# Performance work log

Measured on AMD Instinct MI355X. Metric: run time of the kernel, lower is better.

The kernel has to match this reference:

```python
import jax, jax.numpy as jnp
import numpy as np

B, S, HIST, D, NH, L = 8, 1024, 128, 1024, 16, 6
SD, TD, AD = 10, 3, 5
DH = D // NH
FF = 4 * D
EPS = 1e-5
SCALE = 1.0 / np.sqrt(DH)


def posenc(T):
    # sinusoidal PE, matches PositionalEncoding (positions start at 0)
    pos = jnp.arange(T, dtype=jnp.float32)[:, None]
    div = jnp.exp(jnp.arange(0, D, 2, dtype=jnp.float32) * (-np.log(10000.0) / D))
    pe = jnp.zeros((T, D), jnp.float32)
    pe = pe.at[:, 0::2].set(jnp.sin(pos * div))
    pe = pe.at[:, 1::2].set(jnp.cos(pos * div))
    return pe


def layernorm(x, g, b):
    m = jnp.mean(x, -1, keepdims=True)
    v = jnp.var(x, -1, keepdims=True)
    return (x - m) * jax.lax.rsqrt(v + EPS) * g + b


def mlp2(u, w1, b1, w2, b2):
    # Linear -> SiLU -> Linear (ConditionEmbedding branch)
    return jax.nn.silu(u @ w1 + b1) @ w2 + b2


def mha(q_in, kv_in, wq, bq, wk, bk, wv, bv, wo, bo, mask):
    Bq, Tq, _ = q_in.shape
    Tk = kv_in.shape[1]
    q = (q_in @ wq + bq).reshape(Bq, Tq, NH, DH)
    k = (kv_in @ wk + bk).reshape(Bq, Tk, NH, DH)
    v = (kv_in @ wv + bv).reshape(Bq, Tk, NH, DH)
    s = jnp.einsum('bthd,bshd->bhts', q, k) * SCALE + mask
    a = jax.nn.softmax(s, axis=-1)
    o = jnp.einsum('bhts,bshd->bthd', a, v).reshape(Bq, Tq, D)
    return o @ wo + bo


def setup_inputs():
    key = jax.random.key(0)
    ki = iter(jax.random.split(key, 64))
    w = lambda *sh: jax.random.normal(next(ki), sh, jnp.float32) * 0.02
    z = lambda *sh: jnp.zeros(sh, jnp.float32)
    inp = {
        'x': jax.random.normal(next(ki), (B, S, SD), jnp.float32),
        't': jax.random.randint(next(ki), (B,), 0, 30, dtype=jnp.int32),
        'target': jax.random.normal(next(ki), (B, TD), jnp.float32),
        'action': jax.random.normal(next(ki), (B, AD), jnp.float32),
        'history': jax.random.normal(next(ki), (B, HIST, SD), jnp.float32),
        'in_w': w(SD, D), 'in_b': z(D),
        't_w1': w(1, D), 't_b1': z(D), 't_w2': w(D, D), 't_b2': z(D),
        'tg_w1': w(TD, D), 'tg_b1': z(D), 'tg_w2': w(D, D), 'tg_b2': z(D),
        'ac_w1': w(AD, D), 'ac_b1': z(D), 'ac_w2': w(D, D), 'ac_b2': z(D),
        'sa_wq': w(L, D, D), 'sa_bq': z(L, D), 'sa_wk': w(L, D, D), 'sa_bk': z(L, D),
        'sa_wv': w(L, D, D), 'sa_bv': z(L, D), 'sa_wo': w(L, D, D), 'sa_bo': z(L, D),
        'ca_wq': w(L, D, D), 'ca_bq': z(L, D), 'ca_wk': w(L, D, D), 'ca_bk': z(L, D),
        'ca_wv': w(L, D, D), 'ca_bv': z(L, D), 'ca_wo': w(L, D, D), 'ca_bo': z(L, D),
        'ln1_g': jnp.ones((L, D), jnp.float32), 'ln1_b': z(L, D),
        'ln2_g': jnp.ones((L, D), jnp.float32), 'ln2_b': z(L, D),
        'ln3_g': jnp.ones((L, D), jnp.float32), 'ln3_b': z(L, D),
        'ff_w1': w(L, D, FF), 'ff_b1': z(L, FF), 'ff_w2': w(L, FF, D), 'ff_b2': z(L, D),
        'out_w': w(D, SD), 'out_b': z(SD),
    }
    return inp


def reference(x, t, target, action, history, in_w, in_b,
              t_w1, t_b1, t_w2, t_b2, tg_w1, tg_b1, tg_w2, tg_b2,
              ac_w1, ac_b1, ac_w2, ac_b2,
              sa_wq, sa_bq, sa_wk, sa_bk, sa_wv, sa_bv, sa_wo, sa_bo,
              ca_wq, ca_bq, ca_wk, ca_bk, ca_wv, ca_bv, ca_wo, ca_bo,
              ln1_g, ln1_b, ln2_g, ln2_b, ln3_g, ln3_b,
              ff_w1, ff_b1, ff_w2, ff_b2, out_w, out_b):
    # embed current traj and history (PE applied to each separately, as in torch code)
    x_emb = x @ in_w + in_b + posenc(S)[None]
    h_emb = history @ in_w + in_b + posenc(HIST)[None]
    # condition embedding: t + target + action branches
    cond = (mlp2(t[:, None].astype(jnp.float32), t_w1, t_b1, t_w2, t_b2)
            + mlp2(target, tg_w1, tg_b1, tg_w2, tg_b2)
            + mlp2(action, ac_w1, ac_b1, ac_w2, ac_b2))
    z = jnp.concatenate([h_emb, x_emb], axis=1) + cond[:, None, :]  # [B, T, D]
    T = HIST + S
    mask = jnp.where(jnp.tril(jnp.ones((T, T), bool)), 0.0, -jnp.inf)[None, None]
    mem = z  # TransformerDecoder memory is the (fixed) input sequence
    for i in range(L):
        # post-LN TransformerDecoderLayer: self-attn, cross-attn, relu FFN
        z = layernorm(z + mha(z, z, sa_wq[i], sa_bq[i], sa_wk[i], sa_bk[i],
                              sa_wv[i], sa_bv[i], sa_wo[i], sa_bo[i], mask), ln1_g[i], ln1_b[i])
        z = layernorm(z + mha(z, mem, ca_wq[i], ca_bq[i], ca_wk[i], ca_bk[i],
                              ca_wv[i], ca_bv[i], ca_wo[i], ca_bo[i], mask), ln2_g[i], ln2_b[i])
        ff = jax.nn.relu(z @ ff_w1[i] + ff_b1[i]) @ ff_w2[i] + ff_b2[i]
        z = layernorm(z + ff, ln3_g[i], ln3_b[i])
    return z[:, -S:, :] @ out_w + out_b
```

## Files before the change

### kernel.cpp

```cpp
#include <hip/hip_runtime.h>
#include <hip/hip_bf16.h>
#include <stdint.h>

#define B_    8
#define S_    1024
#define HIST_ 128
#define T_    1152
#define D_    1024
#define NH_   16
#define DH_   64
#define FF_   4096
#define L_    6
#define NROWS_ (B_*T_)

typedef __attribute__((ext_vector_type(8))) __bf16 bf16x8;
typedef __attribute__((ext_vector_type(4))) __bf16 bf16x4;
typedef __attribute__((ext_vector_type(4))) float  f32x4;

static __device__ __forceinline__ f32x4 mfma16(bf16x8 a, bf16x8 b, f32x4 c) {
  return __builtin_amdgcn_mfma_f32_16x16x32_bf16(a, b, c, 0, 0, 0);
}
static __device__ __forceinline__ void gload16(const __bf16* g, __bf16* l) {
  __builtin_amdgcn_global_load_lds((const __attribute__((address_space(1))) void*)g,
                                   (__attribute__((address_space(3))) void*)l, 16, 0, 0);
}
static __device__ __forceinline__ void gload16b(const char* g, char* l) {
  __builtin_amdgcn_global_load_lds((const __attribute__((address_space(1))) void*)g,
                                   (__attribute__((address_space(3))) void*)l, 16, 0, 0);
}
static __device__ __forceinline__ int xcd_swz(int orig, int nwg) {
  const int q = nwg >> 3, r = nwg & 7;
  const int x = orig & 7, i = orig >> 3;
  return (x < r ? x*(q+1) : r*(q+1) + (x-r)*q) + i;
}

template<int OUTMODE, int RELU>
__global__ __launch_bounds__(512, 2) void gemm256_k(const __bf16* __restrict__ A,
                                                    const __bf16* __restrict__ Bt,
                                                    const float* __restrict__ b1,
                                                    const float* __restrict__ b2,
                                                    const float* __restrict__ b3, int s1, int s2,
                                                    void* __restrict__ CoutRM,
                                                    __bf16* __restrict__ CoutT,
                                                    int M, int N, int K, int ldc, int tsplit) {
  __shared__ __align__(16) __bf16 Lds[2][2][2][8192];
  const int tid = threadIdx.x;
  const int wid = tid >> 6, ln = tid & 63;
  const int wm = wid >> 2, wn = wid & 3;
  const int l15 = ln & 15, g = ln >> 4;
  const int nbx = N >> 8;
  const int wg = xcd_swz(blockIdx.x, gridDim.x);
  const int m0 = (wg / nbx) << 8, n0 = (wg % nbx) << 8;
  const size_t rstep = (size_t)K * 2;

  const int srow = tid >> 2, schunk = tid & 3;
  const int sx = (schunk ^ ((srow >> 1) & 3)) << 4;
  const char* gAr = (const char*)A  + (size_t)(m0 + srow)*rstep + sx;
  const char* gBr = (const char*)Bt + (size_t)(n0 + srow)*rstep + sx;
  const size_t hstep = (size_t)128 * rstep;

  const int xr = (g ^ ((l15 >> 1) & 3)) << 4;
  const int arow = l15 * 64 + xr;
  const int aoffm = (wm*128 + 0) * 64;
  const int boff  = (wn*64) * 64;

  const f32x4 zero = {0.f,0.f,0.f,0.f};
  f32x4 acc[8][4];
#pragma unroll
  for (int i=0;i<8;i++)
#pragma unroll
    for (int j=0;j<4;j++) acc[i][j] = zero;

  auto stage4 = [&](int buf, int ks, int tile) {
    const size_t off = (size_t)tile*128 + (size_t)ks*64;
    char* la = (char*)&Lds[buf][ks][0][0];
    char* lb = (char*)&Lds[buf][ks][1][0];
    gload16b(gAr + off,         la + tid*16);
    gload16b(gAr + off + hstep, la + 8192 + tid*16);
    gload16b(gBr + off,         lb + tid*16);
    gload16b(gBr + off + hstep, lb + 8192 + tid*16);
  };

  auto ktile = [&](int buf, bool st, int stile, bool gate0) {
    if (gate0) { asm volatile("s_waitcnt vmcnt(0)" ::: "memory"); }
    else       { asm volatile("s_waitcnt vmcnt(8)" ::: "memory"); }
    __builtin_amdgcn_s_barrier();
    const char* As0 = (const char*)&Lds[buf][0][0][0];
    const char* Bs0 = (const char*)&Lds[buf][0][1][0];
    const char* As1 = (const char*)&Lds[buf][1][0][0];
    const char* Bs1 = (const char*)&Lds[buf][1][1][0];
    bf16x8 af[4], af2[4], bfr[4];
#pragma unroll
    for (int mi=0;mi<4;mi++) af[mi]  = *(const bf16x8*)(As0 + aoffm + mi*1024 + arow);
#pragma unroll
    for (int ni=0;ni<4;ni++) bfr[ni] = *(const bf16x8*)(Bs0 + boff + ni*1024 + arow);
    __builtin_amdgcn_s_setprio(1);
#pragma unroll
    for (int mi=0;mi<4;mi++)
#pragma unroll
      for (int ni=0;ni<4;ni++) acc[mi][ni] = mfma16(af[mi], bfr[ni], acc[mi][ni]);
    __builtin_amdgcn_s_setprio(0);
#pragma unroll
    for (int mi=0;mi<4;mi++) af2[mi] = *(const bf16x8*)(As0 + aoffm + 4096 + mi*1024 + arow);
    asm volatile("s_waitcnt lgkmcnt(0)" ::: "memory");
    __builtin_amdgcn_sched_barrier(0);
    __builtin_amdgcn_s_barrier();
    if (st) stage4(buf, 0, stile);
    __builtin_amdgcn_s_setprio(1);
#pragma unroll
    for (int mi=0;mi<4;mi++)
#pragma unroll
      for (int ni=0;ni<4;ni++) acc[4+mi][ni] = mfma16(af2[mi], bfr[ni], acc[4+mi][ni]);
    __builtin_amdgcn_s_setprio(0);
#pragma unroll
    for (int mi=0;mi<4;mi++) af[mi]  = *(const bf16x8*)(As1 + aoffm + mi*1024 + arow);
#pragma unroll
    for (int ni=0;ni<4;ni++) bfr[ni] = *(const bf16x8*)(Bs1 + boff + ni*1024 + arow);
    __builtin_amdgcn_s_setprio(1);
#pragma unroll
    for (int mi=0;mi<4;mi++)
#pragma unroll
      for (int ni=0;ni<4;ni++) acc[mi][ni] = mfma16(af[mi], bfr[ni], acc[mi][ni]);
    __builtin_amdgcn_s_setprio(0);
#pragma unroll
    for (int mi=0;mi<4;mi++) af2[mi] = *(const bf16x8*)(As1 + aoffm + 4096 + mi*1024 + arow);
    asm volatile("s_waitcnt lgkmcnt(0)" ::: "memory");
    __builtin_amdgcn_sched_barrier(0);
    __builtin_amdgcn_s_barrier();
    if (st) stage4(buf, 1, stile);
    __builtin_amdgcn_s_setprio(1);
#pragma unroll
    for (int mi=0;mi<4;mi++)
#pragma unroll
      for (int ni=0;ni<4;ni++) acc[4+mi][ni] = mfma16(af2[mi], bfr[ni], acc[4+mi][ni]);
    __builtin_amdgcn_s_setprio(0);
  };

  stage4(0, 0, 0); stage4(0, 1, 0);
  stage4(1, 0, 1); stage4(1, 1, 1);

  const int NT = K >> 6, NI = NT >> 1;
  for (int i = 0; i < NI; ++i) {
    const bool st = (i + 1 < NI);
    ktile(0, st, 2*i + 2, false);
    ktile(1, st, 2*i + 3, i == NI - 1);
  }

  const int colb = n0 + wn*64 + l15;
#pragma unroll
  for (int mi=0;mi<8;mi++) {
    const int row = m0 + wm*128 + mi*16 + g*4;
#pragma unroll
    for (int ni=0;ni<4;ni++) {
      const int col = colb + ni*16;
      const float bv = (col < s1) ? b1[col] : ((col < s2) ? b2[col-s1] : b3[col-s2]);
      if (OUTMODE == 3 && col >= tsplit) {
        bf16x4 ct;
#pragma unroll
        for (int j=0;j<4;j++) {
          float v = acc[mi][ni][j] + bv;
          if (RELU) v = fmaxf(v, 0.f);
          ct[j] = (__bf16)v;
        }
        *(bf16x4*)(CoutT + (size_t)(col - tsplit)*M + row) = ct;
      } else {
#pragma unroll
        for (int j=0;j<4;j++) {
          float v = acc[mi][ni][j] + bv;
          if (RELU) v = fmaxf(v, 0.f);
          if (OUTMODE == 0) ((float*)CoutRM)[(size_t)(row+j)*ldc + col] = v;
          else              ((__bf16*)CoutRM)[(size_t)(row+j)*ldc + col] = (__bf16)v;
        }
      }
    }
  }
}

__global__ __launch_bounds__(256) void attn_k(const __bf16* __restrict__ QK,
                                              const __bf16* __restrict__ Vt,
                                              __bf16* __restrict__ O) {
  __shared__ __align__(16) __bf16 Ks[2][4096];
  __shared__ __align__(16) __bf16 Vs[2][4096];
  __shared__ __align__(16) __bf16 Pl[4][32*72];
  const int tid = threadIdx.x;
  const int wv = tid >> 6, ln = tid & 63;
  const int l15 = ln & 15, g = ln >> 4;
  const int wg = xcd_swz(blockIdx.x, 1152);
  const int qb = 8 - (wg % 9);
  const int hd = (wg / 9) & 15;
  const int b  = wg / 144;
  const int q0 = qb*128 + wv*32;

  bf16x8 qf[2][2];
#pragma unroll
  for (int f=0; f<2; ++f)
#pragma unroll
    for (int h=0; h<2; ++h)
      qf[f][h] = *(const bf16x8*)(QK + (size_t)(b*T_ + q0 + f*16 + l15)*2048 + hd*64 + h*32 + g*8);

  const int sr = tid >> 3;
  const int si = tid & 7;
  const int cb0 = (si*16) ^ ((sr & 7) << 4);
  const char* kg = (const char*)(QK + (size_t)b*T_*2048 + 1024 + hd*64);
  const char* vg = (const char*)(Vt + (size_t)hd*64*NROWS_ + (size_t)b*T_);

  const f32x4 zero = {0.f,0.f,0.f,0.f};
  f32x4 o[2][4];
#pragma unroll
  for (int f=0; f<2; ++f)
#pragma unroll
    for (int d=0; d<4; ++d) o[f][d] = zero;
  float mrun[2] = {-3.0e38f, -3.0e38f};
  float lrun[2] = {0.f, 0.f};
  const int nt = 2*qb + 2;

  {
    const int c = 0, kt = 0;
#pragma unroll
    for (int hr=0; hr<2; ++hr) {
      const int r = sr + hr*32;
      gload16((const __bf16*)(kg + (size_t)(kt + r)*4096 + cb0), &Ks[c][0] + hr*2048 + wv*512);
      gload16((const __bf16*)(vg + (size_t)r*(NROWS_*2) + (size_t)kt*2 + cb0), &Vs[c][0] + hr*2048 + wv*512);
    }
  }

  for (int t = 0; t < nt; ++t) {
    __syncthreads();
    if (t+1 < nt) {
      const int c = (t+1)&1, kt2 = (t+1)*64;
#pragma unroll
      for (int hr=0; hr<2; ++hr) {
        const int r = sr + hr*32;
        gload16((const __bf16*)(kg + (size_t)(kt2 + r)*4096 + cb0), &Ks[c][0] + hr*2048 + wv*512);
        gload16((const __bf16*)(vg + (size_t)r*(NROWS_*2) + (size_t)kt2*2 + cb0), &Vs[c][0] + hr*2048 + wv*512);
      }
    }
    const int kt = t*64;
    if (kt > q0 + 31) continue;
    const char* ks = (const char*)&Ks[t&1][0];
    const char* vs = (const char*)&Vs[t&1][0];

#pragma unroll
    for (int f=0; f<2; ++f) {
      const int qrow = q0 + f*16 + l15;
      f32x4 st[4];
      __builtin_amdgcn_s_setprio(1);
#pragma unroll
      for (int kf=0; kf<4; ++kf) {
        const int row = kf*16 + l15;
        const int swz = (row & 7) << 4;
        const bf16x8 k0 = *(const bf16x8*)(ks + row*128 + ((g*16) ^ swz));
        const bf16x8 k1 = *(const bf16x8*)(ks + row*128 + ((64 + g*16) ^ swz));
        st[kf] = mfma16(k1, qf[f][1], mfma16(k0, qf[f][0], zero));
      }
      __builtin_amdgcn_s_setprio(0);
      float p[16];
#pragma unroll
      for (int kf=0; kf<4; ++kf)
#pragma unroll
        for (int r=0; r<4; ++r) {
          const int kgl = kt + kf*16 + g*4 + r;
          p[kf*4+r] = (kgl <= qrow) ? st[kf][r]*0.125f : -3.0e38f;
        }
      float mloc = p[0];
#pragma unroll
      for (int i=1;i<16;i++) mloc = fmaxf(mloc, p[i]);
      mloc = fmaxf(mloc, __shfl_xor(mloc, 16));
      mloc = fmaxf(mloc, __shfl_xor(mloc, 32));
      const float mnew = fmaxf(mrun[f], mloc);
      const float corr = __expf(mrun[f] - mnew);
      float ls = 0.f;
#pragma unroll
      for (int i=0;i<16;i++) { p[i] = __expf(p[i] - mnew); ls += p[i]; }
      ls += __shfl_xor(ls, 16); ls += __shfl_xor(ls, 32);
      lrun[f] = lrun[f]*corr + ls;
      mrun[f] = mnew;
#pragma unroll
      for (int kf=0; kf<4; ++kf) {
        bf16x4 pw;
#pragma unroll
        for (int r=0;r<4;r++) pw[r] = (__bf16)p[kf*4+r];
        *(bf16x4*)(&Pl[wv][(f*16 + l15)*72 + kf*16 + g*4]) = pw;
      }
      float cr[4];
#pragma unroll
      for (int r=0;r<4;r++) cr[r] = __shfl(corr, g*4 + r);
#pragma unroll
      for (int db=0; db<4; ++db)
#pragma unroll
        for (int r=0;r<4;r++) o[f][db][r] *= cr[r];
    }
    __builtin_amdgcn_s_setprio(1);
#pragma unroll
    for (int f=0; f<2; ++f)
#pragma unroll
      for (int ks2=0; ks2<2; ++ks2) {
        const bf16x8 pa = *(const bf16x8*)(&Pl[wv][(f*16 + l15)*72 + ks2*32 + g*8]);
#pragma unroll
        for (int db=0; db<4; ++db) {
          const int d = db*16 + l15;
          const bf16x8 vf = *(const bf16x8*)(vs + d*128 + ((ks2*64 + g*16) ^ ((d & 7) << 4)));
          o[f][db] = mfma16(pa, vf, o[f][db]);
        }
      }
    __builtin_amdgcn_s_setprio(0);
  }

#pragma unroll
  for (int f=0; f<2; ++f) {
    const float inv = 1.f / lrun[f];
    float ir[4];
#pragma unroll
    for (int r=0;r<4;r++) ir[r] = __shfl(inv, g*4 + r);
#pragma unroll
    for (int db=0; db<4; ++db)
#pragma unroll
      for (int r=0;r<4;r++)
        O[(size_t)(b*T_ + q0 + f*16 + g*4 + r)*D_ + hd*64 + db*16 + l15] = (__bf16)(o[f][db][r]*ir[r]);
  }
}

__global__ __launch_bounds__(256) void wprep_k(const float* __restrict__ q, const float* __restrict__ k,
                                               const float* __restrict__ v, const float* __restrict__ o,
                                               const float* __restrict__ cq, const float* __restrict__ ck,
                                               const float* __restrict__ cv, const float* __restrict__ co,
                                               const float* __restrict__ f1, const float* __restrict__ f2,
                                               __bf16* __restrict__ wb) {
  __shared__ float tile[32][33];
  const int id = blockIdx.x;
  const float* src; __bf16* dst; int R, C, bx, by;
  if (id < 8192) {
    const int m = id >> 10, t = id & 1023; bx = t & 31; by = t >> 5;
    const float* srcs[8] = {q,k,v,o,cq,ck,cv,co};
    src = srcs[m]; dst = wb + (size_t)m*1048576; R = 1024; C = 1024;
  } else if (id < 12288) {
    const int t = id - 8192; bx = t & 127; by = t >> 7;
    src = f1; dst = wb + (size_t)8*1048576; R = 1024; C = 4096;
  } else {
    const int t = id - 12288; bx = t & 31; by = t >> 5;
    src = f2; dst = wb + (size_t)12*1048576; R = 4096; C = 1024;
  }
  const int tx = threadIdx.x & 31, ty = threadIdx.x >> 5;
  const int r0 = by*32, c0 = bx*32;
#pragma unroll
  for (int i=0;i<4;i++) tile[ty+i*8][tx] = src[(size_t)(r0+ty+i*8)*C + c0+tx];
  __syncthreads();
#pragma unroll
  for (int i=0;i<4;i++) dst[(size_t)(c0+ty+i*8)*R + r0+tx] = (__bf16)tile[tx][ty+i*8];
}

__global__ __launch_bounds__(256) void ln_k(const float* __restrict__ zin, const float* __restrict__ yin,
                                            const float* __restrict__ gam, const float* __restrict__ bet,
                                            float* __restrict__ zout, __bf16* __restrict__ zbout) {
  const int row = blockIdx.x, tid = threadIdx.x;
  const f32x4 zv = ((const f32x4*)(zin + (size_t)row*D_))[tid];
  const f32x4 yv = ((const f32x4*)(yin + (size_t)row*D_))[tid];
  f32x4 v = zv + yv;
  float s1 = v[0]+v[1]+v[2]+v[3];
  float s2 = v[0]*v[0]+v[1]*v[1]+v[2]*v[2]+v[3]*v[3];
#pragma unroll
  for (int off=32; off; off>>=1) { s1 += __shfl_xor(s1,off); s2 += __shfl_xor(s2,off); }
  __shared__ float red[8];
  const int wv = tid>>6, ln = tid&63;
  if (ln==0) { red[wv] = s1; red[4+wv] = s2; }
  __syncthreads();
  s1 = red[0]+red[1]+red[2]+red[3];
  s2 = red[4]+red[5]+red[6]+red[7];
  const float mean = s1 * (1.f/1024.f);
  const float var = s2 * (1.f/1024.f) - mean*mean;
  const float rs = rsqrtf(var + 1e-5f);
  const f32x4 gv = ((const f32x4*)gam)[tid];
  const f32x4 bv = ((const f32x4*)bet)[tid];
  f32x4 r; bf16x4 rb;
#pragma unroll
  for (int j=0;j<4;j++) { float t = (v[j]-mean)*rs*gv[j] + bv[j]; r[j] = t; rb[j] = (__bf16)t; }
  ((f32x4*)(zout + (size_t)row*D_))[tid] = r;
  ((bf16x4*)(zbout + (size_t)row*D_))[tid] = rb;
}

__global__ __launch_bounds__(256) void cond1_k(const int* __restrict__ t, const float* __restrict__ target,
                                               const float* __restrict__ action,
                                               const float* __restrict__ t_w1, const float* __restrict__ t_b1,
                                               const float* __restrict__ tg_w1, const float* __restrict__ tg_b1,
                                               const float* __restrict__ ac_w1, const float* __restrict__ ac_b1,
                                               float* __restrict__ h3) {
  const int i = blockIdx.x*256 + threadIdx.x;
  const int b = i >> 10, d = i & 1023;
  float u = (float)t[b] * t_w1[d] + t_b1[d];
  h3[i] = u / (1.f + __expf(-u));
  u = tg_b1[d];
#pragma unroll
  for (int j=0;j<3;j++) u += target[b*3+j]*tg_w1[j*1024+d];
  h3[8192 + i] = u / (1.f + __expf(-u));
  u = ac_b1[d];
#pragma unroll
  for (int j=0;j<5;j++) u += action[b*5+j]*ac_w1[j*1024+d];
  h3[16384 + i] = u / (1.f + __expf(-u));
}

__global__ __launch_bounds__(256) void cond2_k(const float* __restrict__ h3,
                                               const float* __restrict__ t_w2, const float* __restrict__ tg_w2,
                                               const float* __restrict__ ac_w2, float* __restrict__ cpart) {
  const int i = blockIdx.x*256 + threadIdx.x;
  const int ks = blockIdx.y;
  const int b = i >> 10, d = i & 1023;
  const float* ht = h3 + b*1024;
  const float* hg = h3 + 8192 + b*1024;
  const float* ha = h3 + 16384 + b*1024;
  float a = 0.f;
  for (int k = ks*128; k < ks*128+128; ++k)
    a += ht[k]*t_w2[(size_t)k*1024+d] + hg[k]*tg_w2[(size_t)k*1024+d] + ha[k]*ac_w2[(size_t)k*1024+d];
  cpart[ks*8192 + i] = a;
}

__global__ __launch_bounds__(256) void embed_k(const float* __restrict__ x, const float* __restrict__ hist,
                                               const float* __restrict__ in_w, const float* __restrict__ in_b,
                                               const float* __restrict__ cpart,
                                               const float* __restrict__ t_b2, const float* __restrict__ tg_b2,
                                               const float* __restrict__ ac_b2,
                                               float* __restrict__ z, __bf16* __restrict__ zb,
                                               __bf16* __restrict__ memb) {
  const int row = blockIdx.x, tid = threadIdx.x;
  const int b = row / T_, tt = row - b*T_;
  const float* feat = (tt < HIST_) ? (hist + ((size_t)b*HIST_ + tt)*10) : (x + ((size_t)b*S_ + (tt-HIST_))*10);
  float f[10];
#pragma unroll
  for (int s=0;s<10;s++) f[s] = feat[s];
  const float te = (float)((tt < HIST_) ? tt : tt - HIST_);
  f32x4 a = ((const f32x4*)in_b)[tid];
#pragma unroll
  for (int u=0;u<2;u++) {
    const int d = tid*4 + 2*u;
    const float freq = __expf((float)d * (-9.210340371976184f/1024.f));
    float sn, cs;
    __sincosf(te*freq, &sn, &cs);
    a[2*u] += sn; a[2*u+1] += cs;
  }
  a += ((const f32x4*)t_b2)[tid];
  a += ((const f32x4*)tg_b2)[tid];
  a += ((const f32x4*)ac_b2)[tid];
  const int cb = b*256 + tid;
#pragma unroll
  for (int ks=0;ks<8;ks++) a += ((const f32x4*)cpart)[ks*2048 + cb];
#pragma unroll
  for (int s=0;s<10;s++) {
    const f32x4 wv = ((const f32x4*)(in_w + s*1024))[tid];
    a += wv * f[s];
  }
  ((f32x4*)(z + (size_t)row*D_))[tid] = a;
  bf16x4 ab;
#pragma unroll
  for (int j=0;j<4;j++) ab[j] = (__bf16)a[j];
  ((bf16x4*)(zb + (size_t)row*D_))[tid] = ab;
  ((bf16x4*)(memb + (size_t)row*D_))[tid] = ab;
}

__global__ __launch_bounds__(256) void outp_k(const float* __restrict__ z, const float* __restrict__ w,
                                              const float* __restrict__ bo, float* __restrict__ out) {
  const int wv = threadIdx.x>>6, ln = threadIdx.x&63;
  const int row = blockIdx.x*4 + wv;
  const int b = row >> 10, s = row & 1023;
  const float* zr = z + ((size_t)b*T_ + HIST_ + s)*D_;
  float acc[10];
#pragma unroll
  for (int o=0;o<10;o++) acc[o]=0.f;
  for (int k=ln; k<1024; k+=64) {
    const float zv = zr[k];
    const float* wr = w + k*10;
#pragma unroll
    for (int o=0;o<10;o++) acc[o] += zv*wr[o];
  }
#pragma unroll
  for (int o=0;o<10;o++) {
#pragma unroll
    for (int off=32; off; off>>=1) acc[o] += __shfl_xor(acc[o], off);
  }
  if (ln==0) {
#pragma unroll
    for (int o=0;o<10;o++) out[(size_t)row*10+o] = acc[o] + bo[o];
  }
}

extern "C" void kernel_launch(void* const* d_in, const int* in_sizes, int n_in,
                              void* d_out, int out_size, void* d_ws, size_t ws_size,
                              hipStream_t stream) {
  const float* x      = (const float*)d_in[0];
  const int*   t      = (const int*)  d_in[1];
  const float* target = (const float*)d_in[2];
  const float* action = (const float*)d_in[3];
  const float* hist   = (const float*)d_in[4];
  const float* in_w   = (const float*)d_in[5];
  const float* in_b   = (const float*)d_in[6];
  const float* t_w1   = (const float*)d_in[7];
  const float* t_b1   = (const float*)d_in[8];
  const float* t_w2   = (const float*)d_in[9];
  const float* t_b2   = (const float*)d_in[10];
  const float* tg_w1  = (const float*)d_in[11];
  const float* tg_b1  = (const float*)d_in[12];
  const float* tg_w2  = (const float*)d_in[13];
  const float* tg_b2  = (const float*)d_in[14];
  const float* ac_w1  = (const float*)d_in[15];
  const float* ac_b1  = (const float*)d_in[16];
  const float* ac_w2  = (const float*)d_in[17];
  const float* ac_b2  = (const float*)d_in[18];
  const float* sa_wq  = (const float*)d_in[19];
  const float* sa_bq  = (const float*)d_in[20];
  const float* sa_wk  = (const float*)d_in[21];
  const float* sa_bk  = (const float*)d_in[22];
  const float* sa_wv  = (const float*)d_in[23];
  const float* sa_bv  = (const float*)d_in[24];
  const float* sa_wo  = (const float*)d_in[25];
  const float* sa_bo  = (const float*)d_in[26];
  const float* ca_wq  = (const float*)d_in[27];
  const float* ca_bq  = (const float*)d_in[28];
  const float* ca_wk  = (const float*)d_in[29];
  const float* ca_bk  = (const float*)d_in[30];
  const float* ca_wv  = (const float*)d_in[31];
  const float* ca_bv  = (const float*)d_in[32];
  const float* ca_wo  = (const float*)d_in[33];
  const float* ca_bo  = (const float*)d_in[34];
  const float* ln1_g  = (const float*)d_in[35];
  const float* ln1_b  = (const float*)d_in[36];
  const float* ln2_g  = (const float*)d_in[37];
  const float* ln2_b  = (const float*)d_in[38];
  const float* ln3_g  = (const float*)d_in[39];
  const float* ln3_b  = (const float*)d_in[40];
  const float* ff_w1  = (const float*)d_in[41];
  const float* ff_b1  = (const float*)d_in[42];
  const float* ff_w2  = (const float*)d_in[43];
  const float* ff_b2  = (const float*)d_in[44];
  const float* out_w  = (const float*)d_in[45];
  const float* out_b  = (const float*)d_in[46];

  if (ws_size < (size_t)224*1024*1024) return;

  char* p = (char*)d_ws;
  auto take = [&](size_t bytes) { char* r = p; p += (bytes + 255) & ~(size_t)255; return r; };
  __bf16* wbuf = (__bf16*)take((size_t)16*1024*1024*2);
  float*  z    = (float*) take((size_t)NROWS_*D_*4);
  __bf16* zb   = (__bf16*)take((size_t)NROWS_*D_*2);
  __bf16* memb = (__bf16*)take((size_t)NROWS_*D_*2);
  __bf16* qk   = (__bf16*)take((size_t)NROWS_*2048*2);
  __bf16* vt   = (__bf16*)take((size_t)1024*NROWS_*2);
  __bf16* ob   = (__bf16*)take((size_t)NROWS_*D_*2);
  float*  y    = (float*) take((size_t)NROWS_*D_*4);
  float*  h3   = (float*) take((size_t)3*8192*4);
  float*  cpart= (float*) take((size_t)8*8192*4);
  __bf16* ffh  = qk;

  const dim3 blk(256);
  const dim3 blk5(512);
  const int BIG = 1<<30;
  cond1_k<<<32, blk, 0, stream>>>(t, target, action, t_w1, t_b1, tg_w1, tg_b1, ac_w1, ac_b1, h3);
  cond2_k<<<dim3(32,8), blk, 0, stream>>>(h3, t_w2, tg_w2, ac_w2, cpart);
  embed_k<<<NROWS_, blk, 0, stream>>>(x, hist, in_w, in_b, cpart, t_b2, tg_b2, ac_b2, z, zb, memb);

  const int M = NROWS_;
  for (int li=0; li<L_; ++li) {
    const size_t w0 = (size_t)li*D_*D_, b0 = (size_t)li*D_;
    const size_t f1 = (size_t)li*D_*FF_, fb1 = (size_t)li*FF_;
    wprep_k<<<16384, blk, 0, stream>>>(sa_wq+w0, sa_wk+w0, sa_wv+w0, sa_wo+w0,
                                       ca_wq+w0, ca_wk+w0, ca_wv+w0, ca_wo+w0,
                                       ff_w1+f1, ff_w2+f1, wbuf);
    gemm256_k<3,0><<<36*12, blk5, 0, stream>>>(zb, wbuf+0*1048576, sa_bq+b0, sa_bk+b0, sa_bv+b0, 1024, 2048,
                                               qk, vt, M, 3072, 1024, 2048, 2048);
    attn_k<<<1152, blk, 0, stream>>>(qk, vt, ob);
    gemm256_k<0,0><<<36*4, blk5, 0, stream>>>(ob, wbuf+3*1048576, sa_bo+b0, sa_bo+b0, sa_bo+b0, BIG, BIG,
                                              y, vt, M, 1024, 1024, 1024, BIG);
    ln_k<<<NROWS_, blk, 0, stream>>>(z, y, ln1_g+b0, ln1_b+b0, z, zb);
    gemm256_k<1,0><<<36*4, blk5, 0, stream>>>(zb, wbuf+4*1048576, ca_bq+b0, ca_bq+b0, ca_bq+b0, BIG, BIG,
                                              qk, vt, M, 1024, 1024, 2048, BIG);
    gemm256_k<3,0><<<36*8, blk5, 0, stream>>>(memb, wbuf+5*1048576, ca_bk+b0, ca_bv+b0, ca_bv+b0, 1024, 2048,
                                              qk + 1024, vt, M, 2048, 1024, 2048, 1024);
    attn_k<<<1152, blk, 0, stream>>>(qk, vt, ob);
    gemm256_k<0,0><<<36*4, blk5, 0, stream>>>(ob, wbuf+7*1048576, ca_bo+b0, ca_bo+b0, ca_bo+b0, BIG, BIG,
                                              y, vt, M, 1024, 1024, 1024, BIG);
    ln_k<<<NROWS_, blk, 0, stream>>>(z, y, ln2_g+b0, ln2_b+b0, z, zb);
    gemm256_k<1,1><<<36*16, blk5, 0, stream>>>(zb, wbuf+(size_t)8*1048576, ff_b1+fb1, ff_b1+fb1, ff_b1+fb1, BIG, BIG,
                                               ffh, vt, M, 4096, 1024, 4096, BIG);
    gemm256_k<0,0><<<36*4, blk5, 0, stream>>>(ffh, wbuf+(size_t)12*1048576, ff_b2+b0, ff_b2+b0, ff_b2+b0, BIG, BIG,
                                              y, vt, M, 1024, 4096, 1024, BIG);
    ln_k<<<NROWS_, blk, 0, stream>>>(z, y, ln3_g+b0, ln3_b+b0, z, zb);
  }
  outp_k<<<2048, blk, 0, stream>>>(z, out_w, out_b, (float*)d_out);
}
```

Baseline: 4.494 ms.

## Fuse cross-attn Q/KV GEMMs, reorder LDS fragment loads, add lazy softmax rescale

The GEMM kernel gains a second A pointer chosen by output column, so the cross-attention Q projection (from zb) and the K/V projection (from memb) run as one N=3072 launch instead of two. The GEMM k-tile loop now loads all A/B fragments for both half-tiles into separate registers ahead of the MFMAs and drops sched_barriers, aiming to overlap LDS reads with compute at the cost of more VGPRs. In attention, when no row's max grows by more than 8, the old max is kept and the output rescale is skipped (lazy rescaling), which cuts exp and multiply work but lets the unnormalised values grow by up to e^8.

```diff
diff --git a/kernel.cpp b/kernel.cpp
--- a/kernel.cpp
+++ b/kernel.cpp
@@ -36,6 +36,7 @@
 
 template<int OUTMODE, int RELU>
 __global__ __launch_bounds__(512, 2) void gemm256_k(const __bf16* __restrict__ A,
+                                                    const __bf16* __restrict__ A2, int asplit,
                                                     const __bf16* __restrict__ Bt,
                                                     const float* __restrict__ b1,
                                                     const float* __restrict__ b2,
@@ -52,16 +53,17 @@
   const int wg = xcd_swz(blockIdx.x, gridDim.x);
   const int m0 = (wg / nbx) << 8, n0 = (wg % nbx) << 8;
   const size_t rstep = (size_t)K * 2;
+  const __bf16* Aeff = (n0 < asplit) ? A : A2;
 
   const int srow = tid >> 2, schunk = tid & 3;
   const int sx = (schunk ^ ((srow >> 1) & 3)) << 4;
-  const char* gAr = (const char*)A  + (size_t)(m0 + srow)*rstep + sx;
-  const char* gBr = (const char*)Bt + (size_t)(n0 + srow)*rstep + sx;
+  const char* gAr = (const char*)Aeff + (size_t)(m0 + srow)*rstep + sx;
+  const char* gBr = (const char*)Bt   + (size_t)(n0 + srow)*rstep + sx;
   const size_t hstep = (size_t)128 * rstep;
 
   const int xr = (g ^ ((l15 >> 1) & 3)) << 4;
   const int arow = l15 * 64 + xr;
-  const int aoffm = (wm*128 + 0) * 64;
+  const int aoffm = (wm*128) * 64;
   const int boff  = (wn*64) * 64;
 
   const f32x4 zero = {0.f,0.f,0.f,0.f};
@@ -89,50 +91,48 @@
     const char* Bs0 = (const char*)&Lds[buf][0][1][0];
     const char* As1 = (const char*)&Lds[buf][1][0][0];
     const char* Bs1 = (const char*)&Lds[buf][1][1][0];
-    bf16x8 af[4], af2[4], bfr[4];
-#pragma unroll
-    for (int mi=0;mi<4;mi++) af[mi]  = *(const bf16x8*)(As0 + aoffm + mi*1024 + arow);
-#pragma unroll
-    for (int ni=0;ni<4;ni++) bfr[ni] = *(const bf16x8*)(Bs0 + boff + ni*1024 + arow);
+    bf16x8 a0[4], a1[4], b0[4], a2[4], b1v[4], a3[4];
+#pragma unroll
+    for (int mi=0;mi<4;mi++) a0[mi] = *(const bf16x8*)(As0 + aoffm + mi*1024 + arow);
+#pragma unroll
+    for (int ni=0;ni<4;ni++) b0[ni] = *(const bf16x8*)(Bs0 + boff + ni*1024 + arow);
+#pragma unroll
+    for (int mi=0;mi<4;mi++) a1[mi] = *(const bf16x8*)(As0 + aoffm + 4096 + mi*1024 + arow);
     __builtin_amdgcn_s_setprio(1);
 #pragma unroll
     for (int mi=0;mi<4;mi++)
 #pragma unroll
-      for (int ni=0;ni<4;ni++) acc[mi][ni] = mfma16(af[mi], bfr[ni], acc[mi][ni]);
+      for (int ni=0;ni<4;ni++) acc[mi][ni] = mfma16(a0[mi], b0[ni], acc[mi][ni]);
     __builtin_amdgcn_s_setprio(0);
 #pragma unroll
-    for (int mi=0;mi<4;mi++) af2[mi] = *(const bf16x8*)(As0 + aoffm + 4096 + mi*1024 + arow);
+    for (int mi=0;mi<4;mi++) a2[mi]  = *(const bf16x8*)(As1 + aoffm + mi*1024 + arow);
+#pragma unroll
+    for (int ni=0;ni<4;ni++) b1v[ni] = *(const bf16x8*)(Bs1 + boff + ni*1024 + arow);
     asm volatile("s_waitcnt lgkmcnt(0)" ::: "memory");
-    __builtin_amdgcn_sched_barrier(0);
     __builtin_amdgcn_s_barrier();
     if (st) stage4(buf, 0, stile);
     __builtin_amdgcn_s_setprio(1);
 #pragma unroll
     for (int mi=0;mi<4;mi++)
 #pragma unroll
-      for (int ni=0;ni<4;ni++) acc[4+mi][ni] = mfma16(af2[mi], bfr[ni], acc[4+mi][ni]);
+      for (int ni=0;ni<4;ni++) acc[4+mi][ni] = mfma16(a1[mi], b0[ni], acc[4+mi][ni]);
     __builtin_amdgcn_s_setprio(0);
 #pragma unroll
-    for (int mi=0;mi<4;mi++) af[mi]  = *(const bf16x8*)(As1 + aoffm + mi*1024 + arow);
-#pragma unroll
-    for (int ni=0;ni<4;ni++) bfr[ni] = *(const bf16x8*)(Bs1 + boff + ni*1024 + arow);
+    for (int mi=0;mi<4;mi++) a3[mi] = *(const bf16x8*)(As1 + aoffm + 4096 + mi*1024 + arow);
     __builtin_amdgcn_s_setprio(1);
 #pragma unroll
     for (int mi=0;mi<4;mi++)
 #pragma unroll
-      for (int ni=0;ni<4;ni++) acc[mi][ni] = mfma16(af[mi], bfr[ni], acc[mi][ni]);
+      for (int ni=0;ni<4;ni++) acc[mi][ni] = mfma16(a2[mi], b1v[ni], acc[mi][ni]);
     __builtin_amdgcn_s_setprio(0);
-#pragma unroll
-    for (int mi=0;mi<4;mi++) af2[mi] = *(const bf16x8*)(As1 + aoffm + 4096 + mi*1024 + arow);
     asm volatile("s_waitcnt lgkmcnt(0)" ::: "memory");
-    __builtin_amdgcn_sched_barrier(0);
     __builtin_amdgcn_s_barrier();
     if (st) stage4(buf, 1, stile);
     __builtin_amdgcn_s_setprio(1);
 #pragma unroll
     for (int mi=0;mi<4;mi++)
 #pragma unroll
-      for (int ni=0;ni<4;ni++) acc[4+mi][ni] = mfma16(af2[mi], bfr[ni], acc[4+mi][ni]);
+      for (int ni=0;ni<4;ni++) acc[4+mi][ni] = mfma16(a3[mi], b1v[ni], acc[4+mi][ni]);
     __builtin_amdgcn_s_setprio(0);
   };
 
@@ -267,14 +267,29 @@
       for (int i=1;i<16;i++) mloc = fmaxf(mloc, p[i]);
       mloc = fmaxf(mloc, __shfl_xor(mloc, 16));
       mloc = fmaxf(mloc, __shfl_xor(mloc, 32));
-      const float mnew = fmaxf(mrun[f], mloc);
-      const float corr = __expf(mrun[f] - mnew);
-      float ls = 0.f;
-#pragma unroll
-      for (int i=0;i<16;i++) { p[i] = __expf(p[i] - mnew); ls += p[i]; }
-      ls += __shfl_xor(ls, 16); ls += __shfl_xor(ls, 32);
-      lrun[f] = lrun[f]*corr + ls;
-      mrun[f] = mnew;
+      if (__all(mloc - mrun[f] <= 8.f)) {
+        float ls = 0.f;
+#pragma unroll
+        for (int i=0;i<16;i++) { p[i] = __expf(p[i] - mrun[f]); ls += p[i]; }
+        ls += __shfl_xor(ls, 16); ls += __shfl_xor(ls, 32);
+        lrun[f] += ls;
+      } else {
+        const float mnew = fmaxf(mrun[f], mloc);
+        const float corr = __expf(mrun[f] - mnew);
+        float ls = 0.f;
+#pragma unroll
+        for (int i=0;i<16;i++) { p[i] = __expf(p[i] - mnew); ls += p[i]; }
+        ls += __shfl_xor(ls, 16); ls += __shfl_xor(ls, 32);
+        lrun[f] = lrun[f]*corr + ls;
+        mrun[f] = mnew;
+        float cr[4];
+#pragma unroll
+        for (int r=0;r<4;r++) cr[r] = __shfl(corr, g*4 + r);
+#pragma unroll
+        for (int db=0; db<4; ++db)
+#pragma unroll
+          for (int r=0;r<4;r++) o[f][db][r] *= cr[r];
+      }
 #pragma unroll
       for (int kf=0; kf<4; ++kf) {
         bf16x4 pw;
@@ -282,13 +297,6 @@
         for (int r=0;r<4;r++) pw[r] = (__bf16)p[kf*4+r];
         *(bf16x4*)(&Pl[wv][(f*16 + l15)*72 + kf*16 + g*4]) = pw;
       }
-      float cr[4];
-#pragma unroll
-      for (int r=0;r<4;r++) cr[r] = __shfl(corr, g*4 + r);
-#pragma unroll
-      for (int db=0; db<4; ++db)
-#pragma unroll
-        for (int r=0;r<4;r++) o[f][db][r] *= cr[r];
     }
     __builtin_amdgcn_s_setprio(1);
 #pragma unroll
@@ -562,23 +570,27 @@
     wprep_k<<<16384, blk, 0, stream>>>(sa_wq+w0, sa_wk+w0, sa_wv+w0, sa_wo+w0,
                                        ca_wq+w0, ca_wk+w0, ca_wv+w0, ca_wo+w0,
                                        ff_w1+f1, ff_w2+f1, wbuf);
-    gemm256_k<3,0><<<36*12, blk5, 0, stream>>>(zb, wbuf+0*1048576, sa_bq+b0, sa_bk+b0, sa_bv+b0, 1024, 2048,
+    gemm256_k<3,0><<<36*12, blk5, 0, stream>>>(zb, zb, BIG, wbuf+0*1048576,
+                                               sa_bq+b0, sa_bk+b0, sa_bv+b0, 1024, 2048,
                                                qk, vt, M, 3072, 1024, 2048, 2048);
     attn_k<<<1152, blk, 0, stream>>>(qk, vt, ob);
-    gemm256_k<0,0><<<36*4, blk5, 0, stream>>>(ob, wbuf+3*1048576, sa_bo+b0, sa_bo+b0, sa_bo+b0, BIG, BIG,
+    gemm256_k<0,0><<<36*4, blk5, 0, stream>>>(ob, ob, BIG, wbuf+3*1048576,
+                                              sa_bo+b0, sa_bo+b0, sa_bo+b0, BIG, BIG,
                                               y, vt, M, 1024, 1024, 1024, BIG);
     ln_k<<<NROWS_, blk, 0, stream>>>(z, y, ln1_g+b0, ln1_b+b0, z, zb);
-    gemm256_k<1,0><<<36*4, blk5, 0, stream>>>(zb, wbuf+4*1048576, ca_bq+b0, ca_bq+b0, ca_bq+b0, BIG, BIG,
-                                              qk, vt, M, 1024, 1024, 2048, BIG);
-    gemm256_k<3,0><<<36*8, blk5, 0, stream>>>(memb, wbuf+5*1048576, ca_bk+b0, ca_bv+b0, ca_bv+b0, 1024, 2048,
-                                              qk + 1024, vt, M, 2048, 1024, 2048, 1024);
+    gemm256_k<3,0><<<36*12, blk5, 0, stream>>>(zb, memb, 1024, wbuf+4*1048576,
+                                               ca_bq+b0, ca_bk+b0, ca_bv+b0, 1024, 2048,
+                                               qk, vt, M, 3072, 1024, 2048, 2048);
     attn_k<<<1152, blk, 0, stream>>>(qk, vt, ob);
-    gemm256_k<0,0><<<36*4, blk5, 0, stream>>>(ob, wbuf+7*1048576, ca_bo+b0, ca_bo+b0, ca_bo+b0, BIG, BIG,
+    gemm256_k<0,0><<<36*4, blk5, 0, stream>>>(ob, ob, BIG, wbuf+7*1048576,
+                                              ca_bo+b0, ca_bo+b0, ca_bo+b0, BIG, BIG,
                                               y, vt, M, 1024, 1024, 1024, BIG);
     ln_k<<<NROWS_, blk, 0, stream>>>(z, y, ln2_g+b0, ln2_b+b0, z, zb);
-    gemm256_k<1,1><<<36*16, blk5, 0, stream>>>(zb, wbuf+(size_t)8*1048576, ff_b1+fb1, ff_b1+fb1, ff_b1+fb1, BIG, BIG,
+    gemm256_k<1,1><<<36*16, blk5, 0, stream>>>(zb, zb, BIG, wbuf+(size_t)8*1048576,
+                                               ff_b1+fb1, ff_b1+fb1, ff_b1+fb1, BIG, BIG,
                                                ffh, vt, M, 4096, 1024, 4096, BIG);
-    gemm256_k<0,0><<<36*4, blk5, 0, stream>>>(ffh, wbuf+(size_t)12*1048576, ff_b2+b0, ff_b2+b0, ff_b2+b0, BIG, BIG,
+    gemm256_k<0,0><<<36*4, blk5, 0, stream>>>(ffh, ffh, BIG, wbuf+(size_t)12*1048576,
+                                              ff_b2+b0, ff_b2+b0, ff_b2+b0, BIG, BIG,
                                               y, vt, M, 1024, 4096, 1024, BIG);
     ln_k<<<NROWS_, blk, 0, stream>>>(z, y, ln3_g+b0, ln3_b+b0, z, zb);
   }
```

New measurement: 4.354 ms. -3.1%, faster.
